# Kernel tuning notes

Measured on AMD Instinct MI355X. Metric: run time of the kernel, lower is better.

The kernel has to match this reference:

```python
import jax, jax.numpy as jnp
import numpy as np

HIDDEN = 1000
DICT = 4811
T = 44
B = 256


def _lstm_cell(x, h, c, W_ih, W_hh, b_ih, b_hh):
    # gates: [B, 4*H], PyTorch order i, f, g, o
    gates = x @ W_ih.T + b_ih + h @ W_hh.T + b_hh
    i, f, g, o = jnp.split(gates, 4, axis=-1)
    i = jax.nn.sigmoid(i)
    f = jax.nn.sigmoid(f)
    g = jnp.tanh(g)
    o = jax.nn.sigmoid(o)
    c_new = f * c + i * g
    h_new = o * jnp.tanh(c_new)
    return h_new, c_new


def setup_inputs() -> dict:
    key = jax.random.key(0)
    ks = jax.random.split(key, 20)
    s = 0.02
    H = HIDDEN
    return {
        "x": jax.random.normal(ks[0], (B, T, H), jnp.float32),
        "h1": jax.random.normal(ks[1], (B, H), jnp.float32),
        "h2": jax.random.normal(ks[2], (B, H), jnp.float32),
        "c1": jax.random.normal(ks[3], (B, H), jnp.float32),
        "c2": jax.random.normal(ks[4], (B, H), jnp.float32),
        "layer_W": jax.random.normal(ks[5], (H, H), jnp.float32) * s,
        "layer_b": jnp.zeros((H,), jnp.float32),
        "W_ih1": jax.random.normal(ks[6], (4 * H, 2 * H), jnp.float32) * s,
        "W_hh1": jax.random.normal(ks[7], (4 * H, H), jnp.float32) * s,
        "b_ih1": jnp.zeros((4 * H,), jnp.float32),
        "b_hh1": jnp.zeros((4 * H,), jnp.float32),
        "W_ih2": jax.random.normal(ks[8], (4 * H, DICT + 2 * H), jnp.float32) * s,
        "W_hh2": jax.random.normal(ks[9], (4 * H, H), jnp.float32) * s,
        "b_ih2": jnp.zeros((4 * H,), jnp.float32),
        "b_hh2": jnp.zeros((4 * H,), jnp.float32),
        "out_W": jax.random.normal(ks[10], (DICT, H), jnp.float32) * s,
        "out_b": jnp.zeros((DICT,), jnp.float32),
    }


def reference(x, h1, h2, c1, c2, layer_W, layer_b,
              W_ih1, W_hh1, b_ih1, b_hh1,
              W_ih2, W_hh2, b_ih2, b_hh2,
              out_W, out_b):
    # input projection: [B, T, H]
    xp = x @ layer_W.T + layer_b
    prev0 = jnp.zeros((x.shape[0], DICT), x.dtype)

    def step(carry, xt):
        h1, c1, h2, c2, prev = carry
        l1_in = jnp.concatenate([xt, h1], axis=1)            # [B, 2H]
        h1n, c1n = _lstm_cell(l1_in, h1, c1, W_ih1, W_hh1, b_ih1, b_hh1)
        l2_in = jnp.concatenate([prev, h2, h1n], axis=1)     # [B, DICT+2H]
        h2n, c2n = _lstm_cell(l2_in, h2, c2, W_ih2, W_hh2, b_ih2, b_hh2)
        logits = h2n @ out_W.T + out_b                       # [B, DICT]
        # NOTE: original torch code softmaxes over dim=0 (batch axis)
        y = jax.nn.softmax(logits, axis=0)
        return (h1n, c1n, h2n, c2n, y), y

    xs = jnp.transpose(xp, (1, 0, 2))                        # [T, B, H]
    _, ys = jax.lax.scan(step, (h1, c1, h2, c2, prev0), xs)
    return jnp.transpose(ys, (1, 0, 2))                      # [B, T, DICT]
```

## Files before the change

kernel.cpp:

```cpp
#include <hip/hip_runtime.h>
#include <hip/hip_bf16.h>

#define HID   1000
#define DICT  4811
#define TT    44
#define BB    256
#define G4    4000
#define G4P   4096
#define K1P   2048
#define K2P   6912
#define HP    1024
#define Z2_H2 4864
#define Z2_H1 5888
#define PD    3
#define GPART ((long long)BB * G4P)

typedef __attribute__((ext_vector_type(8))) short short8;
typedef __attribute__((ext_vector_type(4))) float f32x4;

__device__ __forceinline__ short f2b(float f) {
    unsigned u = __float_as_uint(f);
    unsigned r = (u + 0x7FFFu + ((u >> 16) & 1u)) >> 16;
    return (short)r;
}

__device__ __forceinline__ void gload16(const void* g, const short* l) {
    __builtin_amdgcn_global_load_lds(
        (const __attribute__((address_space(1))) unsigned int*)g,
        (__attribute__((address_space(3))) unsigned int*)l, 16, 0, 0);
}

__global__ void prep_w1i(const float* __restrict__ wih1, const float* __restrict__ whh1,
                         short* __restrict__ w) {
    for (size_t i = (size_t)blockIdx.x * blockDim.x + threadIdx.x; i < (size_t)G4P * K1P;
         i += (size_t)gridDim.x * blockDim.x) {
        int n = (int)(i >> 11), j = (int)(i & 2047);
        int h = n >> 2, g = n & 3;
        float v = 0.f;
        if (h < HID) {
            int r = g * HID + h;
            if (j < HID) v = wih1[(size_t)r * 2000 + j];
            else if (j >= 1024 && j < 1024 + HID) {
                int jj = j - 1024;
                v = wih1[(size_t)r * 2000 + HID + jj] + whh1[(size_t)r * HID + jj];
            }
        }
        w[i] = f2b(v);
    }
}

__global__ void prep_w2p(const float* __restrict__ wih2, const float* __restrict__ whh2,
                         short* __restrict__ w) {
    int n = blockIdx.y;
    int j = blockIdx.x * 256 + threadIdx.x;
    float v = 0.f;
    if (n < G4) {
        if (j < DICT) v = wih2[(size_t)n * 6811 + j];
        else if (j >= Z2_H2 && j < Z2_H2 + HID) {
            int jj = j - Z2_H2;
            v = wih2[(size_t)n * 6811 + DICT + jj] + whh2[(size_t)n * HID + jj];
        } else if (j >= Z2_H1 && j < Z2_H1 + HID) {
            int jj = j - Z2_H1;
            v = wih2[(size_t)n * 6811 + DICT + HID + jj];
        }
    }
    w[(size_t)n * K2P + j] = f2b(v);
}

__global__ void prep_outwp(const float* __restrict__ outw, short* __restrict__ w) {
    int n = blockIdx.y;
    int j = blockIdx.x * 256 + threadIdx.x;
    float v = (n < DICT && j < HID) ? outw[(size_t)n * HID + j] : 0.f;
    w[(size_t)n * HP + j] = f2b(v);
}

__global__ void prep_cvt(const float* __restrict__ src, short* __restrict__ dst, size_t n) {
    for (size_t i = (size_t)blockIdx.x * blockDim.x + threadIdx.x; i < n;
         i += (size_t)gridDim.x * blockDim.x)
        dst[i] = f2b(src[i]);
}

__global__ void prep_addv(const float* __restrict__ a, const float* __restrict__ b,
                          float* __restrict__ dst, int n) {
    int i = blockIdx.x * blockDim.x + threadIdx.x;
    if (i < n) dst[i] = a[i] + b[i];
}

__global__ void prep_biasi(const float* __restrict__ bi, const float* __restrict__ bh,
                           float* __restrict__ dst) {
    int n = blockIdx.x * 256 + threadIdx.x;
    if (n >= 4096) return;
    int h = n >> 2, g = n & 3;
    dst[n] = (h < HID) ? bi[g * HID + h] + bh[g * HID + h] : 0.f;
}

__global__ void init_vec(const float* __restrict__ src, short* __restrict__ dst, int ld) {
    int i = blockIdx.x * blockDim.x + threadIdx.x;
    if (i >= BB * HID) return;
    int b = i / HID, h = i % HID;
    dst[(size_t)b * ld + h] = f2b(src[i]);
}

template <int EPI, int AF32>
__global__ __launch_bounds__(256) void gemm_nt(
    const void* __restrict__ Ap, int lda,
    const short* __restrict__ Bp, int ldb,
    const float* __restrict__ bias,
    void* __restrict__ Cp, long long partStride, int ldc,
    int M, int N, int Kvalid)
{
    __shared__ short As[64][40];
    __shared__ short Bs[64][40];
    const int tid  = threadIdx.x;
    const int lane = tid & 63;
    const int wave = tid >> 6;
    const int wm = wave >> 1, wn = wave & 1;
    const int tm = blockIdx.y * 64, tn = blockIdx.x * 64;
    const int srow = tid >> 2;
    const int scol = (tid & 3) * 8;

    const int nk = (Kvalid + 31) >> 5;
    const int s0 = (int)(((long long)nk * blockIdx.z) / gridDim.z);
    const int s1 = (int)(((long long)nk * (blockIdx.z + 1)) / gridDim.z);

    const int arow = tm + srow;
    const int brow = tn + srow;
    const bool bvalid = brow < N;

    auto loadA = [&](int ks) -> short8 {
        int k = (ks << 5) + scol;
        short8 r = {0, 0, 0, 0, 0, 0, 0, 0};
        if (k + 8 <= Kvalid) {
            if (AF32) {
                const f32x4* p = (const f32x4*)((const float*)Ap + (size_t)arow * lda + k);
                f32x4 u0 = p[0], u1 = p[1];
                r[0] = f2b(u0[0]); r[1] = f2b(u0[1]); r[2] = f2b(u0[2]); r[3] = f2b(u0[3]);
                r[4] = f2b(u1[0]); r[5] = f2b(u1[1]); r[6] = f2b(u1[2]); r[7] = f2b(u1[3]);
            } else {
                r = *(const short8*)((const short*)Ap + (size_t)arow * lda + k);
            }
        }
        return r;
    };
    auto loadB = [&](int ks) -> short8 {
        int k = (ks << 5) + scol;
        short8 r = {0, 0, 0, 0, 0, 0, 0, 0};
        if (bvalid && (k + 8 <= Kvalid))
            r = *(const short8*)(Bp + (size_t)brow * ldb + k);
        return r;
    };

    f32x4 acc[2][2];
    for (int a = 0; a < 2; ++a)
        for (int b = 0; b < 2; ++b)
            acc[a][b] = (f32x4){0.f, 0.f, 0.f, 0.f};

    short8 ra = loadA(s0), rb = loadB(s0);
    *(short8*)&As[srow][scol] = ra;
    *(short8*)&Bs[srow][scol] = rb;
    __syncthreads();

    const int kg = (lane >> 4) * 8;
    const int fr = lane & 15;

    for (int s = s0; s < s1; ++s) {
        short8 a0 = *(short8*)&As[wm * 32 + fr][kg];
        short8 a1 = *(short8*)&As[wm * 32 + 16 + fr][kg];
        short8 b0 = *(short8*)&Bs[wn * 32 + fr][kg];
        short8 b1 = *(short8*)&Bs[wn * 32 + 16 + fr][kg];
        short8 na, nb;
        if (s + 1 < s1) { na = loadA(s + 1); nb = loadB(s + 1); }
        acc[0][0] = __builtin_amdgcn_mfma_f32_16x16x32_bf16(a0, b0, acc[0][0], 0, 0, 0);
        acc[0][1] = __builtin_amdgcn_mfma_f32_16x16x32_bf16(a0, b1, acc[0][1], 0, 0, 0);
        acc[1][0] = __builtin_amdgcn_mfma_f32_16x16x32_bf16(a1, b0, acc[1][0], 0, 0, 0);
        acc[1][1] = __builtin_amdgcn_mfma_f32_16x16x32_bf16(a1, b1, acc[1][1], 0, 0, 0);
        __syncthreads();
        if (s + 1 < s1) {
            *(short8*)&As[srow][scol] = na;
            *(short8*)&Bs[srow][scol] = nb;
        }
        __syncthreads();
    }

    float* Cf = (float*)Cp + (size_t)partStride * blockIdx.z;
    for (int mi = 0; mi < 2; ++mi)
        for (int ni = 0; ni < 2; ++ni) {
            int col = tn + wn * 32 + ni * 16 + (lane & 15);
            if (col >= N) continue;
            float bv = bias ? bias[col] : 0.f;
            int row0 = tm + wm * 32 + mi * 16 + ((lane >> 4) << 2);
            f32x4 v = acc[mi][ni];
            for (int j = 0; j < 4; ++j) {
                int row = row0 + j;
                float val = v[j] + bv;
                if (EPI == 0) {
                    Cf[(size_t)row * ldc + col] = val;
                } else {
                    int b = row / TT, t = row % TT;
                    ((short*)Cp)[((size_t)t * BB + b) * ldc + col] = f2b(val);
                }
            }
        }
}

__global__ __launch_bounds__(256) void gates1F(
    const short* __restrict__ xp_t,
    const short* __restrict__ h1m,
    const short* __restrict__ w1i,
    const f32x4* __restrict__ bias4,
    float* __restrict__ c1,
    short* __restrict__ zh1,
    short* __restrict__ h1nxt)
{
    __shared__ __align__(16) short smem[PD][4096];
    const int tid  = threadIdx.x;
    const int lane = tid & 63;
    const int w    = tid >> 6;
    const int wm = w >> 1, wn = w & 1;
    const int tm = blockIdx.y * 64;
    const int tn = blockIdx.x * 64;
    const int nk = K1P / 32;

    const int rA = tid >> 2, sl = tid & 3;
    const int swz = (sl ^ ((rA >> 1) & 3)) << 3;
    const size_t aoff = (size_t)(tm + rA) * HP + (size_t)swz;
    const size_t boff = (size_t)(tn + rA) * K1P + (size_t)swz;

    auto stage = [&](int buf, int s) {
        const int k0 = s << 5;
        const short* As = (k0 < 1024) ? xp_t : h1m;
        const short* l = &smem[buf][0];
        gload16(As + k0 + aoff, l + tid * 8);
        gload16(w1i + k0 + boff, l + 2048 + tid * 8);
    };

    const int fr = lane & 15;
    const int kg = lane >> 4;
    int aRd[2], bRd[2];
    #pragma unroll
    for (int mi = 0; mi < 2; ++mi) {
        int row = wm * 32 + mi * 16 + fr;
        aRd[mi] = row * 32 + ((kg ^ ((row >> 1) & 3)) << 3);
    }
    #pragma unroll
    for (int ni = 0; ni < 2; ++ni) {
        int row = wn * 32 + ni * 16 + fr;
        bRd[ni] = 2048 + row * 32 + ((kg ^ ((row >> 1) & 3)) << 3);
    }

    f32x4 acc[2][2];
    #pragma unroll
    for (int a = 0; a < 2; ++a)
        #pragma unroll
        for (int b = 0; b < 2; ++b)
            acc[a][b] = (f32x4){0.f, 0.f, 0.f, 0.f};

    #pragma unroll
    for (int i = 0; i < PD; ++i) stage(i, i);

    int buf = 0;
    for (int s = 0; s < nk; ++s) {
        const int ahead = nk - 1 - s;
        if (ahead >= 2)      asm volatile("s_waitcnt vmcnt(4)" ::: "memory");
        else if (ahead == 1) asm volatile("s_waitcnt vmcnt(2)" ::: "memory");
        else                 asm volatile("s_waitcnt vmcnt(0)" ::: "memory");
        __builtin_amdgcn_s_barrier();

        const short* bp = &smem[buf][0];
        short8 af[2], bf[2];
        #pragma unroll
        for (int i = 0; i < 2; ++i) af[i] = *(const short8*)(bp + aRd[i]);
        #pragma unroll
        for (int i = 0; i < 2; ++i) bf[i] = *(const short8*)(bp + bRd[i]);
        asm volatile("s_waitcnt lgkmcnt(0)" ::: "memory");
        __builtin_amdgcn_sched_barrier(0);
        __builtin_amdgcn_s_barrier();
        if (s + PD < nk) stage(buf, s + PD);

        #pragma unroll
        for (int mi = 0; mi < 2; ++mi)
            #pragma unroll
            for (int ni = 0; ni < 2; ++ni)
                acc[mi][ni] = __builtin_amdgcn_mfma_f32_16x16x32_bf16(af[mi], bf[ni], acc[mi][ni], 0, 0, 0);

        buf = (buf + 1 == PD) ? 0 : buf + 1;
    }

    float* gl = (float*)&smem[0][0];
    #pragma unroll
    for (int mi = 0; mi < 2; ++mi)
        #pragma unroll
        for (int ni = 0; ni < 2; ++ni) {
            int row = wm * 32 + mi * 16 + kg * 4;
            int col = wn * 32 + ni * 16 + fr;
            #pragma unroll
            for (int j = 0; j < 4; ++j)
                gl[(row + j) * 68 + col] = acc[mi][ni][j];
        }
    __syncthreads();

    const int b_loc = tid & 63;
    const int b_g = tm + b_loc;
    #pragma unroll
    for (int q = 0; q < 4; ++q) {
        int h_loc = (tid >> 6) * 4 + q;
        int h_g = blockIdx.x * 16 + h_loc;
        if (h_g >= HID) continue;
        f32x4 g4 = *(const f32x4*)(gl + b_loc * 68 + h_loc * 4);
        g4 += bias4[h_g];
        float ii = 1.f / (1.f + expf(-g4[0]));
        float ff = 1.f / (1.f + expf(-g4[1]));
        float tg = tanhf(g4[2]);
        float oo = 1.f / (1.f + expf(-g4[3]));
        float cn = ff * c1[(size_t)b_g * HID + h_g] + ii * tg;
        c1[(size_t)b_g * HID + h_g] = cn;
        short hb = f2b(oo * tanhf(cn));
        zh1[(size_t)b_g * K2P + h_g] = hb;
        h1nxt[(size_t)b_g * HP + h_g] = hb;
    }
}

__global__ __launch_bounds__(512, 4) void gemm_s128(
    const short* __restrict__ A0, const short* __restrict__ A1, int splitA, int lda,
    const short* __restrict__ Bw, int ldb,
    float* __restrict__ C, long long partStride, int ldc, int nk)
{
    __shared__ __align__(16) short smem[PD][8192];
    const int tid  = threadIdx.x;
    const int lane = tid & 63;
    const int w    = tid >> 6;
    const int wm = w >> 2, wn = w & 3;
    const int tm = blockIdx.y * 128;
    const int tn = blockIdx.x * 128;
    const int s0 = (int)(((long long)nk * blockIdx.z) / gridDim.z);
    const int s1 = (int)(((long long)nk * (blockIdx.z + 1)) / gridDim.z);

    const int rA = tid >> 2, slA = tid & 3;
    const int swz = (slA ^ ((rA >> 1) & 3)) << 3;
    const size_t aoff = (size_t)(tm + rA) * lda + (size_t)swz;
    const size_t boff = (size_t)(tn + rA) * ldb + (size_t)swz;

    auto stage = [&](int buf, int s) {
        const int k0 = s << 5;
        const short* As = (k0 < splitA) ? A0 : A1;
        const short* l = &smem[buf][0];
        gload16(As + k0 + aoff, l + tid * 8);
        gload16(Bw + k0 + boff, l + 4096 + tid * 8);
    };

    const int fr = lane & 15;
    const int kg = lane >> 4;
    int aRd[4], bRd[2];
    #pragma unroll
    for (int mi = 0; mi < 4; ++mi) {
        int row = wm * 64 + mi * 16 + fr;
        aRd[mi] = row * 32 + ((kg ^ ((row >> 1) & 3)) << 3);
    }
    #pragma unroll
    for (int ni = 0; ni < 2; ++ni) {
        int row = wn * 32 + ni * 16 + fr;
        bRd[ni] = 4096 + row * 32 + ((kg ^ ((row >> 1) & 3)) << 3);
    }

    f32x4 acc[4][2];
    #pragma unroll
    for (int a = 0; a < 4; ++a)
        #pragma unroll
        for (int b = 0; b < 2; ++b)
            acc[a][b] = (f32x4){0.f, 0.f, 0.f, 0.f};

    #pragma unroll
    for (int i = 0; i < PD; ++i)
        if (s0 + i < s1) stage(i, s0 + i);

    int buf = 0;
    for (int s = s0; s < s1; ++s) {
        const int ahead = s1 - 1 - s;
        if (ahead >= 2)      asm volatile("s_waitcnt vmcnt(4)" ::: "memory");
        else if (ahead == 1) asm volatile("s_waitcnt vmcnt(2)" ::: "memory");
        else                 asm volatile("s_waitcnt vmcnt(0)" ::: "memory");
        __builtin_amdgcn_s_barrier();

        const short* bp = &smem[buf][0];
        short8 af[4], bf[2];
        #pragma unroll
        for (int i = 0; i < 4; ++i) af[i] = *(const short8*)(bp + aRd[i]);
        #pragma unroll
        for (int i = 0; i < 2; ++i) bf[i] = *(const short8*)(bp + bRd[i]);
        asm volatile("s_waitcnt lgkmcnt(0)" ::: "memory");
        __builtin_amdgcn_sched_barrier(0);
        __builtin_amdgcn_s_barrier();
        if (s + PD < s1) stage(buf, s + PD);

        #pragma unroll
        for (int mi = 0; mi < 4; ++mi)
            #pragma unroll
            for (int ni = 0; ni < 2; ++ni)
                acc[mi][ni] = __builtin_amdgcn_mfma_f32_16x16x32_bf16(af[mi], bf[ni], acc[mi][ni], 0, 0, 0);

        buf = (buf + 1 == PD) ? 0 : buf + 1;
    }

    float* Cp = C + (size_t)partStride * blockIdx.z;
    const int colb = tn + wn * 32 + fr;
    const int rowb = tm + wm * 64 + (kg << 2);
    #pragma unroll
    for (int mi = 0; mi < 4; ++mi)
        #pragma unroll
        for (int ni = 0; ni < 2; ++ni) {
            int col = colb + ni * 16;
            int row0 = rowb + mi * 16;
            #pragma unroll
            for (int j = 0; j < 4; ++j)
                Cp[(size_t)(row0 + j) * ldc + col] = acc[mi][ni][j];
        }
}

__global__ __launch_bounds__(512) void logits_sm(
    const short* __restrict__ A , const short* __restrict__ Bw ,
    const float* __restrict__ outb, float* __restrict__ out,
    short* __restrict__ z2, int t)
{
    __shared__ __align__(16) short smem[PD][10240];
    __shared__ float red[256];
    const int tid  = threadIdx.x;
    const int lane = tid & 63;
    const int w    = tid >> 6;
    const int wm = w >> 1, wn = w & 1;
    const int tn = blockIdx.x * 64;
    const int nk = HP / 32;

    const int cA0 = w * 64 + lane;
    const int cA1 = cA0 + 512;
    const int rA0 = cA0 >> 2, rA1 = cA1 >> 2;
    const size_t aoff0 = (size_t)rA0 * HP + (size_t)((((cA0 & 3) ^ ((rA0 >> 1) & 3))) << 3);
    const size_t aoff1 = (size_t)rA1 * HP + (size_t)((((cA1 & 3) ^ ((rA1 >> 1) & 3))) << 3);
    const int cB = w * 32 + (lane & 31);
    const int rB = cB >> 2;
    const size_t boff = (size_t)(tn + rB) * HP + (size_t)((((cB & 3) ^ ((rB >> 1) & 3))) << 3);

    auto stage = [&](int buf, int s) {
        const int k0 = s << 5;
        const short* l = &smem[buf][0];
        gload16(A + k0 + aoff0, l + w * 512);
        gload16(A + k0 + aoff1, l + 4096 + w * 512);
        if (lane < 32) gload16(Bw + k0 + boff, l + 8192 + w * 256);
    };

    const int fr = lane & 15;
    const int kg = lane >> 4;
    int aRd[4], bRd[2];
    #pragma unroll
    for (int mi = 0; mi < 4; ++mi) {
        int row = wm * 64 + mi * 16 + fr;
        aRd[mi] = row * 32 + ((kg ^ ((row >> 1) & 3)) << 3);
    }
    #pragma unroll
    for (int ni = 0; ni < 2; ++ni) {
        int row = wn * 32 + ni * 16 + fr;
        bRd[ni] = 8192 + row * 32 + ((kg ^ ((row >> 1) & 3)) << 3);
    }

    f32x4 acc[4][2];
    #pragma unroll
    for (int a = 0; a < 4; ++a)
        #pragma unroll
        for (int b = 0; b < 2; ++b)
            acc[a][b] = (f32x4){0.f, 0.f, 0.f, 0.f};

    #pragma unroll
    for (int i = 0; i < PD; ++i) stage(i, i);

    int buf = 0;
    for (int s = 0; s < nk; ++s) {
        const int ahead = nk - 1 - s;
        if (ahead >= 2)      asm volatile("s_waitcnt vmcnt(6)" ::: "memory");
        else if (ahead == 1) asm volatile("s_waitcnt vmcnt(3)" ::: "memory");
        else                 asm volatile("s_waitcnt vmcnt(0)" ::: "memory");
        __builtin_amdgcn_s_barrier();

        const short* bp = &smem[buf][0];
        short8 af[4], bf[2];
        #pragma unroll
        for (int i = 0; i < 4; ++i) af[i] = *(const short8*)(bp + aRd[i]);
        #pragma unroll
        for (int i = 0; i < 2; ++i) bf[i] = *(const short8*)(bp + bRd[i]);
        asm volatile("s_waitcnt lgkmcnt(0)" ::: "memory");
        __builtin_amdgcn_sched_barrier(0);
        __builtin_amdgcn_s_barrier();
        if (s + PD < nk) stage(buf, s + PD);

        #pragma unroll
        for (int mi = 0; mi < 4; ++mi)
            #pragma unroll
            for (int ni = 0; ni < 2; ++ni)
                acc[mi][ni] = __builtin_amdgcn_mfma_f32_16x16x32_bf16(af[mi], bf[ni], acc[mi][ni], 0, 0, 0);

        buf = (buf + 1 == PD) ? 0 : buf + 1;
    }

    int   colv[2];
    float bv[2];
    #pragma unroll
    for (int ni = 0; ni < 2; ++ni) {
        colv[ni] = tn + wn * 32 + ni * 16 + fr;
        bv[ni] = (colv[ni] < DICT) ? outb[colv[ni]] : 0.f;
    }
    float v[4][2][4];
    float mx[2] = {-3e38f, -3e38f};
    #pragma unroll
    for (int mi = 0; mi < 4; ++mi)
        #pragma unroll
        for (int ni = 0; ni < 2; ++ni)
            #pragma unroll
            for (int j = 0; j < 4; ++j) {
                float x = acc[mi][ni][j] + bv[ni];
                v[mi][ni][j] = x;
                mx[ni] = fmaxf(mx[ni], x);
            }
    #pragma unroll
    for (int ni = 0; ni < 2; ++ni) {
        mx[ni] = fmaxf(mx[ni], __shfl_xor(mx[ni], 16));
        mx[ni] = fmaxf(mx[ni], __shfl_xor(mx[ni], 32));
    }
    if (lane < 16) {
        red[wm * 64 + wn * 32 + fr]      = mx[0];
        red[wm * 64 + wn * 32 + 16 + fr] = mx[1];
    }
    __syncthreads();
    float m[2];
    #pragma unroll
    for (int ni = 0; ni < 2; ++ni) {
        int cc = wn * 32 + ni * 16 + fr;
        m[ni] = fmaxf(fmaxf(red[cc], red[64 + cc]), fmaxf(red[128 + cc], red[192 + cc]));
    }
    __syncthreads();
    float s2[2] = {0.f, 0.f};
    #pragma unroll
    for (int mi = 0; mi < 4; ++mi)
        #pragma unroll
        for (int ni = 0; ni < 2; ++ni)
            #pragma unroll
            for (int j = 0; j < 4; ++j) {
                float e = expf(v[mi][ni][j] - m[ni]);
                v[mi][ni][j] = e;
                s2[ni] += e;
            }
    #pragma unroll
    for (int ni = 0; ni < 2; ++ni) {
        s2[ni] += __shfl_xor(s2[ni], 16);
        s2[ni] += __shfl_xor(s2[ni], 32);
    }
    if (lane < 16) {
        red[wm * 64 + wn * 32 + fr]      = s2[0];
        red[wm * 64 + wn * 32 + 16 + fr] = s2[1];
    }
    __syncthreads();
    float inv[2];
    #pragma unroll
    for (int ni = 0; ni < 2; ++ni) {
        int cc = wn * 32 + ni * 16 + fr;
        inv[ni] = 1.f / (red[cc] + red[64 + cc] + red[128 + cc] + red[192 + cc]);
    }
    const int rowb = wm * 64 + (kg << 2);
    #pragma unroll
    for (int mi = 0; mi < 4; ++mi)
        #pragma unroll
        for (int j = 0; j < 4; ++j) {
            int b = rowb + mi * 16 + j;
            #pragma unroll
            for (int ni = 0; ni < 2; ++ni) {
                if (colv[ni] < DICT) {
                    float y = v[mi][ni][j] * inv[ni];
                    out[(size_t)b * ((size_t)TT * DICT) + (size_t)t * DICT + colv[ni]] = y;
                    z2[(size_t)b * K2P + colv[ni]] = f2b(y);
                }
            }
        }
}

template <int NP>
__global__ void lstm_ewN(const float* __restrict__ g, long long ps,
                         const float* __restrict__ bias, float* __restrict__ c,
                         short* __restrict__ d1, int ld1,
                         short* __restrict__ d2, int ld2)
{
    int i = blockIdx.x * blockDim.x + threadIdx.x;
    if (i >= BB * HID) return;
    int b = i / HID, h = i % HID;
    size_t base = (size_t)b * G4P + h;
    float gi = bias[h], gf = bias[HID + h], gg = bias[2 * HID + h], go = bias[3 * HID + h];
    #pragma unroll
    for (int p = 0; p < NP; ++p) {
        const float* gp = g + (size_t)ps * p + base;
        gi += gp[0];
        gf += gp[HID];
        gg += gp[2 * HID];
        go += gp[3 * HID];
    }
    float ii = 1.f / (1.f + expf(-gi));
    float ff = 1.f / (1.f + expf(-gf));
    float tg = tanhf(gg);
    float oo = 1.f / (1.f + expf(-go));
    float cn = ff * c[i] + ii * tg;
    c[i] = cn;
    float hn = oo * tanhf(cn);
    short hb = f2b(hn);
    d1[(size_t)b * ld1 + h] = hb;
    d2[(size_t)b * ld2 + h] = hb;
}

extern "C" void kernel_launch(void* const* d_in, const int* in_sizes, int n_in,
                              void* d_out, int out_size, void* d_ws, size_t ws_size,
                              hipStream_t stream)
{
    const float* x    = (const float*)d_in[0];
    const float* h1   = (const float*)d_in[1];
    const float* h2   = (const float*)d_in[2];
    const float* c1in = (const float*)d_in[3];
    const float* c2in = (const float*)d_in[4];
    const float* layW = (const float*)d_in[5];
    const float* layb = (const float*)d_in[6];
    const float* Wih1 = (const float*)d_in[7];
    const float* Whh1 = (const float*)d_in[8];
    const float* bih1 = (const float*)d_in[9];
    const float* bhh1 = (const float*)d_in[10];
    const float* Wih2 = (const float*)d_in[11];
    const float* Whh2 = (const float*)d_in[12];
    const float* bih2 = (const float*)d_in[13];
    const float* bhh2 = (const float*)d_in[14];
    const float* outW = (const float*)d_in[15];
    const float* outb = (const float*)d_in[16];
    float* out = (float*)d_out;
    (void)in_sizes; (void)n_in; (void)out_size; (void)ws_size;

    char* ws = (char*)d_ws;
    size_t off = 0;
    auto alloc = [&](size_t bytes) -> void* {
        size_t p = off;
        off = (off + bytes + 255) & ~(size_t)255;
        return (void*)(ws + p);
    };

    short* w1i   = (short*)alloc((size_t)G4P * K1P * 2);
    short* w2cat = (short*)alloc((size_t)G4P * K2P * 2);
    short* outwb = (short*)alloc((size_t)4864 * HP * 2);
    short* laywb = (short*)alloc((size_t)HID * HID * 2);
    short* xp    = (short*)alloc((size_t)TT * BB * HP * 2);
    short* h1A   = (short*)alloc((size_t)BB * HP * 2);
    short* h1B   = (short*)alloc((size_t)BB * HP * 2);
    short* h2pad = (short*)alloc((size_t)BB * HP * 2);
    short* z2    = (short*)alloc((size_t)BB * K2P * 2);
    float* gbuf  = (float*)alloc((size_t)4 * BB * G4P * 4);
    float* c1    = (float*)alloc((size_t)BB * HID * 4);
    float* c2    = (float*)alloc((size_t)BB * HID * 4);
    float* bi1   = (float*)alloc((size_t)G4P * 4);
    float* bias2 = (float*)alloc((size_t)G4 * 4);

    hipMemsetAsync(xp, 0, (size_t)TT * BB * HP * 2, stream);
    hipMemsetAsync(z2, 0, (size_t)BB * K2P * 2, stream);
    hipMemsetAsync(h1A, 0, (size_t)BB * HP * 2, stream);
    hipMemsetAsync(h1B, 0, (size_t)BB * HP * 2, stream);
    hipMemsetAsync(h2pad, 0, (size_t)BB * HP * 2, stream);

    prep_w1i<<<4096, 256, 0, stream>>>(Wih1, Whh1, w1i);
    prep_w2p<<<dim3(27, G4P), 256, 0, stream>>>(Wih2, Whh2, w2cat);
    prep_outwp<<<dim3(4, 4864), 256, 0, stream>>>(outW, outwb);
    prep_cvt<<<1024, 256, 0, stream>>>(layW, laywb, (size_t)HID * HID);
    prep_biasi<<<16, 256, 0, stream>>>(bih1, bhh1, bi1);
    prep_addv<<<16, 256, 0, stream>>>(bih2, bhh2, bias2, G4);
    init_vec<<<1000, 256, 0, stream>>>(h1, h1A, HP);
    init_vec<<<1000, 256, 0, stream>>>(h2, h2pad, HP);
    init_vec<<<1000, 256, 0, stream>>>(h2, z2 + Z2_H2, K2P);
    hipMemcpyAsync(c1, c1in, (size_t)BB * HID * 4, hipMemcpyDeviceToDevice, stream);
    hipMemcpyAsync(c2, c2in, (size_t)BB * HID * 4, hipMemcpyDeviceToDevice, stream);

    gemm_nt<1, 1><<<dim3(16, (BB * TT) / 64, 1), 256, 0, stream>>>(
        x, HID, laywb, HID, layb, xp, 0, HP, BB * TT, HID, HID);

    for (int t = 0; t < TT; ++t) {
        short* hcur = (t & 1) ? h1B : h1A;
        short* hnxt = (t & 1) ? h1A : h1B;

        gates1F<<<dim3(64, 4), 256, 0, stream>>>(
            xp + (size_t)t * BB * HP, hcur - HP, w1i,
            (const f32x4*)bi1, c1, z2 + Z2_H1, hnxt);

        gemm_s128<<<dim3(32, 2, 4), 512, 0, stream>>>(
            z2, z2, 0, K2P, w2cat, K2P, gbuf, GPART, G4P, K2P / 32);
        lstm_ewN<4><<<1000, 256, 0, stream>>>(
            gbuf, GPART, bias2, c2, z2 + Z2_H2, K2P, h2pad, HP);

        logits_sm<<<76, 512, 0, stream>>>(h2pad, outwb, outb, out, z2, t);
    }
}
```

Measured before the change: 3.541 ms.

## Prefetch next LDS fragments during MFMA and double split-K for layer-2 gates

Result: slower. 3.947 ms (+11.5%).

```diff
diff --git a/kernel.cpp b/kernel.cpp
--- a/kernel.cpp
+++ b/kernel.cpp
@@ -256,34 +256,52 @@
             acc[a][b] = (f32x4){0.f, 0.f, 0.f, 0.f};
 
     #pragma unroll
-    for (int i = 0; i < PD; ++i) stage(i, i);
+    for (int i = 0; i < PD; ++i)
+        if (i < nk) stage(i, i);
+
+    asm volatile("s_waitcnt vmcnt(4)" ::: "memory");
+    __builtin_amdgcn_s_barrier();
+    short8 af[2], bf[2];
+    {
+        const short* bp = &smem[0][0];
+        #pragma unroll
+        for (int i = 0; i < 2; ++i) af[i] = *(const short8*)(bp + aRd[i]);
+        #pragma unroll
+        for (int i = 0; i < 2; ++i) bf[i] = *(const short8*)(bp + bRd[i]);
+    }
 
     int buf = 0;
     for (int s = 0; s < nk; ++s) {
-        const int ahead = nk - 1 - s;
-        if (ahead >= 2)      asm volatile("s_waitcnt vmcnt(4)" ::: "memory");
-        else if (ahead == 1) asm volatile("s_waitcnt vmcnt(2)" ::: "memory");
-        else                 asm volatile("s_waitcnt vmcnt(0)" ::: "memory");
-        __builtin_amdgcn_s_barrier();
-
-        const short* bp = &smem[buf][0];
-        short8 af[2], bf[2];
-        #pragma unroll
-        for (int i = 0; i < 2; ++i) af[i] = *(const short8*)(bp + aRd[i]);
-        #pragma unroll
-        for (int i = 0; i < 2; ++i) bf[i] = *(const short8*)(bp + bRd[i]);
         asm volatile("s_waitcnt lgkmcnt(0)" ::: "memory");
         __builtin_amdgcn_sched_barrier(0);
         __builtin_amdgcn_s_barrier();
         if (s + PD < nk) stage(buf, s + PD);
-
+        const int nbuf = (buf + 1 == PD) ? 0 : buf + 1;
+        short8 naf[2], nbf[2];
+        const bool more = (s + 1 < nk);
+        if (more) {
+            int ahead = nk - 1 - (s + 1); if (ahead > PD - 1) ahead = PD - 1;
+            if (ahead >= 2)      asm volatile("s_waitcnt vmcnt(4)" ::: "memory");
+            else if (ahead == 1) asm volatile("s_waitcnt vmcnt(2)" ::: "memory");
+            else                 asm volatile("s_waitcnt vmcnt(0)" ::: "memory");
+            __builtin_amdgcn_s_barrier();
+            const short* np = &smem[nbuf][0];
+            #pragma unroll
+            for (int i = 0; i < 2; ++i) naf[i] = *(const short8*)(np + aRd[i]);
+            #pragma unroll
+            for (int i = 0; i < 2; ++i) nbf[i] = *(const short8*)(np + bRd[i]);
+            __builtin_amdgcn_sched_barrier(0);
+        }
         #pragma unroll
         for (int mi = 0; mi < 2; ++mi)
             #pragma unroll
             for (int ni = 0; ni < 2; ++ni)
                 acc[mi][ni] = __builtin_amdgcn_mfma_f32_16x16x32_bf16(af[mi], bf[ni], acc[mi][ni], 0, 0, 0);
-
-        buf = (buf + 1 == PD) ? 0 : buf + 1;
+        if (more) {
+            #pragma unroll
+            for (int i = 0; i < 2; ++i) { af[i] = naf[i]; bf[i] = nbf[i]; }
+        }
+        buf = nbuf;
     }
 
     float* gl = (float*)&smem[0][0];
@@ -373,32 +391,56 @@
     for (int i = 0; i < PD; ++i)
         if (s0 + i < s1) stage(i, s0 + i);
 
-    int buf = 0;
-    for (int s = s0; s < s1; ++s) {
-        const int ahead = s1 - 1 - s;
+    {
+        int ahead = s1 - 1 - s0; if (ahead > PD - 1) ahead = PD - 1;
         if (ahead >= 2)      asm volatile("s_waitcnt vmcnt(4)" ::: "memory");
         else if (ahead == 1) asm volatile("s_waitcnt vmcnt(2)" ::: "memory");
         else                 asm volatile("s_waitcnt vmcnt(0)" ::: "memory");
-        __builtin_amdgcn_s_barrier();
-
-        const short* bp = &smem[buf][0];
-        short8 af[4], bf[2];
+    }
+    __builtin_amdgcn_s_barrier();
+    short8 af[4], bf[2];
+    {
+        const short* bp = &smem[0][0];
         #pragma unroll
         for (int i = 0; i < 4; ++i) af[i] = *(const short8*)(bp + aRd[i]);
         #pragma unroll
         for (int i = 0; i < 2; ++i) bf[i] = *(const short8*)(bp + bRd[i]);
+    }
+
+    int buf = 0;
+    for (int s = s0; s < s1; ++s) {
         asm volatile("s_waitcnt lgkmcnt(0)" ::: "memory");
         __builtin_amdgcn_sched_barrier(0);
         __builtin_amdgcn_s_barrier();
         if (s + PD < s1) stage(buf, s + PD);
-
+        const int nbuf = (buf + 1 == PD) ? 0 : buf + 1;
+        short8 naf[4], nbf[2];
+        const bool more = (s + 1 < s1);
+        if (more) {
+            int ahead = s1 - 1 - (s + 1); if (ahead > PD - 1) ahead = PD - 1;
+            if (ahead >= 2)      asm volatile("s_waitcnt vmcnt(4)" ::: "memory");
+            else if (ahead == 1) asm volatile("s_waitcnt vmcnt(2)" ::: "memory");
+            else                 asm volatile("s_waitcnt vmcnt(0)" ::: "memory");
+            __builtin_amdgcn_s_barrier();
+            const short* np = &smem[nbuf][0];
+            #pragma unroll
+            for (int i = 0; i < 4; ++i) naf[i] = *(const short8*)(np + aRd[i]);
+            #pragma unroll
+            for (int i = 0; i < 2; ++i) nbf[i] = *(const short8*)(np + bRd[i]);
+            __builtin_amdgcn_sched_barrier(0);
+        }
         #pragma unroll
         for (int mi = 0; mi < 4; ++mi)
             #pragma unroll
             for (int ni = 0; ni < 2; ++ni)
                 acc[mi][ni] = __builtin_amdgcn_mfma_f32_16x16x32_bf16(af[mi], bf[ni], acc[mi][ni], 0, 0, 0);
-
-        buf = (buf + 1 == PD) ? 0 : buf + 1;
+        if (more) {
+            #pragma unroll
+            for (int i = 0; i < 4; ++i) af[i] = naf[i];
+            #pragma unroll
+            for (int i = 0; i < 2; ++i) bf[i] = nbf[i];
+        }
+        buf = nbuf;
     }
 
     float* Cp = C + (size_t)partStride * blockIdx.z;
@@ -471,32 +513,51 @@
     #pragma unroll
     for (int i = 0; i < PD; ++i) stage(i, i);
 
+    asm volatile("s_waitcnt vmcnt(6)" ::: "memory");
+    __builtin_amdgcn_s_barrier();
+    short8 af[4], bf[2];
+    {
+        const short* bp = &smem[0][0];
+        #pragma unroll
+        for (int i = 0; i < 4; ++i) af[i] = *(const short8*)(bp + aRd[i]);
+        #pragma unroll
+        for (int i = 0; i < 2; ++i) bf[i] = *(const short8*)(bp + bRd[i]);
+    }
+
     int buf = 0;
     for (int s = 0; s < nk; ++s) {
-        const int ahead = nk - 1 - s;
-        if (ahead >= 2)      asm volatile("s_waitcnt vmcnt(6)" ::: "memory");
-        else if (ahead == 1) asm volatile("s_waitcnt vmcnt(3)" ::: "memory");
-        else                 asm volatile("s_waitcnt vmcnt(0)" ::: "memory");
-        __builtin_amdgcn_s_barrier();
-
-        const short* bp = &smem[buf][0];
-        short8 af[4], bf[2];
-        #pragma unroll
-        for (int i = 0; i < 4; ++i) af[i] = *(const short8*)(bp + aRd[i]);
-        #pragma unroll
-        for (int i = 0; i < 2; ++i) bf[i] = *(const short8*)(bp + bRd[i]);
         asm volatile("s_waitcnt lgkmcnt(0)" ::: "memory");
         __builtin_amdgcn_sched_barrier(0);
         __builtin_amdgcn_s_barrier();
         if (s + PD < nk) stage(buf, s + PD);
-
+        const int nbuf = (buf + 1 == PD) ? 0 : buf + 1;
+        short8 naf[4], nbf[2];
+        const bool more = (s + 1 < nk);
+        if (more) {
+            int ahead = nk - 1 - (s + 1); if (ahead > PD - 1) ahead = PD - 1;
+            if (ahead >= 2)      asm volatile("s_waitcnt vmcnt(6)" ::: "memory");
+            else if (ahead == 1) asm volatile("s_waitcnt vmcnt(3)" ::: "memory");
+            else                 asm volatile("s_waitcnt vmcnt(0)" ::: "memory");
+            __builtin_amdgcn_s_barrier();
+            const short* np = &smem[nbuf][0];
+            #pragma unroll
+            for (int i = 0; i < 4; ++i) naf[i] = *(const short8*)(np + aRd[i]);
+            #pragma unroll
+            for (int i = 0; i < 2; ++i) nbf[i] = *(const short8*)(np + bRd[i]);
+            __builtin_amdgcn_sched_barrier(0);
+        }
         #pragma unroll
         for (int mi = 0; mi < 4; ++mi)
             #pragma unroll
             for (int ni = 0; ni < 2; ++ni)
                 acc[mi][ni] = __builtin_amdgcn_mfma_f32_16x16x32_bf16(af[mi], bf[ni], acc[mi][ni], 0, 0, 0);
-
-        buf = (buf + 1 == PD) ? 0 : buf + 1;
+        if (more) {
+            #pragma unroll
+            for (int i = 0; i < 4; ++i) af[i] = naf[i];
+            #pragma unroll
+            for (int i = 0; i < 2; ++i) bf[i] = nbf[i];
+        }
+        buf = nbuf;
     }
 
     int   colv[2];
@@ -651,7 +712,7 @@
     short* h1B   = (short*)alloc((size_t)BB * HP * 2);
     short* h2pad = (short*)alloc((size_t)BB * HP * 2);
     short* z2    = (short*)alloc((size_t)BB * K2P * 2);
-    float* gbuf  = (float*)alloc((size_t)4 * BB * G4P * 4);
+    float* gbuf  = (float*)alloc((size_t)8 * BB * G4P * 4);
     float* c1    = (float*)alloc((size_t)BB * HID * 4);
     float* c2    = (float*)alloc((size_t)BB * HID * 4);
     float* bi1   = (float*)alloc((size_t)G4P * 4);
@@ -686,9 +747,9 @@
             xp + (size_t)t * BB * HP, hcur - HP, w1i,
             (const f32x4*)bi1, c1, z2 + Z2_H1, hnxt);
 
-        gemm_s128<<<dim3(32, 2, 4), 512, 0, stream>>>(
+        gemm_s128<<<dim3(32, 2, 8), 512, 0, stream>>>(
             z2, z2, 0, K2P, w2cat, K2P, gbuf, GPART, G4P, K2P / 32);
-        lstm_ewN<4><<<1000, 256, 0, stream>>>(
+        lstm_ewN<8><<<1000, 256, 0, stream>>>(
             gbuf, GPART, bias2, c2, z2 + Z2_H2, K2P, h2pad, HP);
 
         logits_sm<<<76, 512, 0, stream>>>(h2pad, outwb, outb, out, z2, t);
```

## Fuse next-step layer-1 LSTM with layer-2 elementwise and raise split-K to 8

Applied to the files above, without the earlier changes.

After: 3.385 ms. 4.4% less time.

```diff
diff --git a/kernel.cpp b/kernel.cpp
--- a/kernel.cpp
+++ b/kernel.cpp
@@ -203,7 +203,7 @@
         }
 }
 
-__global__ __launch_bounds__(256) void gates1F(
+__device__ __forceinline__ void gates1F_dev(short* smem, int bx, int by,
     const short* __restrict__ xp_t,
     const short* __restrict__ h1m,
     const short* __restrict__ w1i,
@@ -212,13 +212,12 @@
     short* __restrict__ zh1,
     short* __restrict__ h1nxt)
 {
-    __shared__ __align__(16) short smem[PD][4096];
     const int tid  = threadIdx.x;
     const int lane = tid & 63;
     const int w    = tid >> 6;
     const int wm = w >> 1, wn = w & 1;
-    const int tm = blockIdx.y * 64;
-    const int tn = blockIdx.x * 64;
+    const int tm = by * 64;
+    const int tn = bx * 64;
     const int nk = K1P / 32;
 
     const int rA = tid >> 2, sl = tid & 3;
@@ -229,7 +228,7 @@
     auto stage = [&](int buf, int s) {
         const int k0 = s << 5;
         const short* As = (k0 < 1024) ? xp_t : h1m;
-        const short* l = &smem[buf][0];
+        const short* l = smem + buf * 4096;
         gload16(As + k0 + aoff, l + tid * 8);
         gload16(w1i + k0 + boff, l + 2048 + tid * 8);
     };
@@ -266,7 +265,7 @@
         else                 asm volatile("s_waitcnt vmcnt(0)" ::: "memory");
         __builtin_amdgcn_s_barrier();
 
-        const short* bp = &smem[buf][0];
+        const short* bp = smem + buf * 4096;
         short8 af[2], bf[2];
         #pragma unroll
         for (int i = 0; i < 2; ++i) af[i] = *(const short8*)(bp + aRd[i]);
@@ -286,7 +285,7 @@
         buf = (buf + 1 == PD) ? 0 : buf + 1;
     }
 
-    float* gl = (float*)&smem[0][0];
+    float* gl = (float*)smem;
     #pragma unroll
     for (int mi = 0; mi < 2; ++mi)
         #pragma unroll
@@ -304,7 +303,7 @@
     #pragma unroll
     for (int q = 0; q < 4; ++q) {
         int h_loc = (tid >> 6) * 4 + q;
-        int h_g = blockIdx.x * 16 + h_loc;
+        int h_g = bx * 16 + h_loc;
         if (h_g >= HID) continue;
         f32x4 g4 = *(const f32x4*)(gl + b_loc * 68 + h_loc * 4);
         g4 += bias4[h_g];
@@ -318,6 +317,59 @@
         zh1[(size_t)b_g * K2P + h_g] = hb;
         h1nxt[(size_t)b_g * HP + h_g] = hb;
     }
+}
+
+__global__ __launch_bounds__(256) void gates1F(
+    const short* __restrict__ xp_t, const short* __restrict__ h1m,
+    const short* __restrict__ w1i, const f32x4* __restrict__ bias4,
+    float* __restrict__ c1, short* __restrict__ zh1, short* __restrict__ h1nxt)
+{
+    __shared__ __align__(16) short smem[PD * 4096];
+    gates1F_dev(smem, blockIdx.x, blockIdx.y, xp_t, h1m, w1i, bias4, c1, zh1, h1nxt);
+}
+
+__device__ __forceinline__ void lstm2_dev(int blk,
+    const float* __restrict__ g, const float* __restrict__ bias, float* __restrict__ c,
+    short* __restrict__ d1, int ld1, short* __restrict__ d2, int ld2)
+{
+    int i = blk * 256 + threadIdx.x;
+    if (i >= BB * HID) return;
+    int b = i / HID, h = i % HID;
+    size_t base = (size_t)b * G4P + h;
+    float gi = bias[h], gf = bias[HID + h], gg = bias[2 * HID + h], go = bias[3 * HID + h];
+    #pragma unroll
+    for (int p = 0; p < 8; ++p) {
+        const float* gp = g + (size_t)GPART * p + base;
+        gi += gp[0];
+        gf += gp[HID];
+        gg += gp[2 * HID];
+        go += gp[3 * HID];
+    }
+    float ii = 1.f / (1.f + expf(-gi));
+    float ff = 1.f / (1.f + expf(-gf));
+    float tg = tanhf(gg);
+    float oo = 1.f / (1.f + expf(-go));
+    float cn = ff * c[i] + ii * tg;
+    c[i] = cn;
+    float hn = oo * tanhf(cn);
+    short hb = f2b(hn);
+    d1[(size_t)b * ld1 + h] = hb;
+    d2[(size_t)b * ld2 + h] = hb;
+}
+
+__global__ __launch_bounds__(256) void fusedC(
+    const short* __restrict__ xp_t1, const short* __restrict__ h1m,
+    const short* __restrict__ w1i, const f32x4* __restrict__ bi1,
+    float* __restrict__ c1, short* __restrict__ zh1, short* __restrict__ h1nxt,
+    const float* __restrict__ gbuf, const float* __restrict__ bias2,
+    float* __restrict__ c2, short* __restrict__ zh2, short* __restrict__ h2pad)
+{
+    __shared__ __align__(16) short smem[PD * 4096];
+    const int x = blockIdx.x;
+    if (x < 256)
+        gates1F_dev(smem, x & 63, x >> 6, xp_t1, h1m, w1i, bi1, c1, zh1, h1nxt);
+    else
+        lstm2_dev(x - 256, gbuf, bias2, c2, zh2, K2P, h2pad, HP);
 }
 
 __global__ __launch_bounds__(512, 4) void gemm_s128(
@@ -577,37 +629,6 @@
                 }
             }
         }
-}
-
-template <int NP>
-__global__ void lstm_ewN(const float* __restrict__ g, long long ps,
-                         const float* __restrict__ bias, float* __restrict__ c,
-                         short* __restrict__ d1, int ld1,
-                         short* __restrict__ d2, int ld2)
-{
-    int i = blockIdx.x * blockDim.x + threadIdx.x;
-    if (i >= BB * HID) return;
-    int b = i / HID, h = i % HID;
-    size_t base = (size_t)b * G4P + h;
-    float gi = bias[h], gf = bias[HID + h], gg = bias[2 * HID + h], go = bias[3 * HID + h];
-    #pragma unroll
-    for (int p = 0; p < NP; ++p) {
-        const float* gp = g + (size_t)ps * p + base;
-        gi += gp[0];
-        gf += gp[HID];
-        gg += gp[2 * HID];
-        go += gp[3 * HID];
-    }
-    float ii = 1.f / (1.f + expf(-gi));
-    float ff = 1.f / (1.f + expf(-gf));
-    float tg = tanhf(gg);
-    float oo = 1.f / (1.f + expf(-go));
-    float cn = ff * c[i] + ii * tg;
-    c[i] = cn;
-    float hn = oo * tanhf(cn);
-    short hb = f2b(hn);
-    d1[(size_t)b * ld1 + h] = hb;
-    d2[(size_t)b * ld2 + h] = hb;
 }
 
 extern "C" void kernel_launch(void* const* d_in, const int* in_sizes, int n_in,
@@ -651,7 +672,7 @@
     short* h1B   = (short*)alloc((size_t)BB * HP * 2);
     short* h2pad = (short*)alloc((size_t)BB * HP * 2);
     short* z2    = (short*)alloc((size_t)BB * K2P * 2);
-    float* gbuf  = (float*)alloc((size_t)4 * BB * G4P * 4);
+    float* gbuf  = (float*)alloc((size_t)8 * BB * G4P * 4);
     float* c1    = (float*)alloc((size_t)BB * HID * 4);
     float* c2    = (float*)alloc((size_t)BB * HID * 4);
     float* bi1   = (float*)alloc((size_t)G4P * 4);
@@ -678,18 +699,21 @@
     gemm_nt<1, 1><<<dim3(16, (BB * TT) / 64, 1), 256, 0, stream>>>(
         x, HID, laywb, HID, layb, xp, 0, HP, BB * TT, HID, HID);
 
+    gates1F<<<dim3(64, 4), 256, 0, stream>>>(
+        xp, h1A - HP, w1i, (const f32x4*)bi1, c1, z2 + Z2_H1, h1B);
+
     for (int t = 0; t < TT; ++t) {
-        short* hcur = (t & 1) ? h1B : h1A;
-        short* hnxt = (t & 1) ? h1A : h1B;
-
-        gates1F<<<dim3(64, 4), 256, 0, stream>>>(
-            xp + (size_t)t * BB * HP, hcur - HP, w1i,
-            (const f32x4*)bi1, c1, z2 + Z2_H1, hnxt);
-
-        gemm_s128<<<dim3(32, 2, 4), 512, 0, stream>>>(
+        short* hcur = (t & 1) ? h1A : h1B;
+        short* hnxt = (t & 1) ? h1B : h1A;
+        int tn1 = (t + 1 < TT) ? (t + 1) : (TT - 1);
+
+        gemm_s128<<<dim3(32, 2, 8), 512, 0, stream>>>(
             z2, z2, 0, K2P, w2cat, K2P, gbuf, GPART, G4P, K2P / 32);
-        lstm_ewN<4><<<1000, 256, 0, stream>>>(
-            gbuf, GPART, bias2, c2, z2 + Z2_H2, K2P, h2pad, HP);
+
+        fusedC<<<1256, 256, 0, stream>>>(
+            xp + (size_t)tn1 * BB * HP, hcur - HP, w1i, (const f32x4*)bi1,
+            c1, z2 + Z2_H1, hnxt,
+            gbuf, bias2, c2, z2 + Z2_H2, h2pad);
 
         logits_sm<<<76, 512, 0, stream>>>(h2pad, outwb, outb, out, z2, t);
     }
```
